# Performance work log

Hardware: AMD Instinct MI355X
Metric: run time of the kernel (lower is better)

Reference implementation:

```python
import jax, jax.numpy as jnp
import numpy as np

# ---- static config (matches init_kwargs / langevin args) ----
B, N, D = 2, 16384, 3
F_DIM = 128      # feature_net.out_channels
H_DIM = 128      # score_net hidden
N_BLOCKS = 2
K = 4            # denoise_knn
NUM_STEPS = 4
STEP_SIZE = 0.2
STEP_DECAY = 0.95

# static sliding-window neighbor indices, computed once (numpy -> constant)
_offsets = np.arange(-(K - 1) // 2, (K - 1) // 2 + 1)
NBR_IDX = np.clip(np.arange(N)[:, None] + _offsets, 0, N - 1)   # (N, K)
NBR_FLAT = NBR_IDX.reshape(-1)                                  # (N*K,)


def setup_inputs() -> dict:
    key = jax.random.key(0)
    ks = jax.random.split(key, 8)
    s = 0.05
    return {
        "pcl_noisy": jax.random.normal(ks[0], (B, N, D), jnp.float32),
        "Wf1": jax.random.normal(ks[1], (D, F_DIM), jnp.float32) * s,
        "bf1": jnp.zeros((F_DIM,), jnp.float32),
        "Wf2": jax.random.normal(ks[2], (F_DIM, F_DIM), jnp.float32) * s,
        "bf2": jnp.zeros((F_DIM,), jnp.float32),
        "W0": jax.random.normal(ks[3], (D + F_DIM, H_DIM), jnp.float32) * s,
        "b0": jnp.zeros((H_DIM,), jnp.float32),
        "Wb": jax.random.normal(ks[4], (N_BLOCKS, H_DIM, H_DIM), jnp.float32) * s,
        "bb": jnp.zeros((N_BLOCKS, H_DIM), jnp.float32),
        "Wo": jax.random.normal(ks[5], (H_DIM, D), jnp.float32) * s,
        "bo": jnp.zeros((D,), jnp.float32),
    }


def _feature_net(pcl, Wf1, bf1, Wf2, bf2):
    # pointwise MLP: (B,N,3) -> (B,N,F)
    h = jax.nn.relu(pcl @ Wf1 + bf1)
    return h @ Wf2 + bf2


def _score_net(x_cent, feat, W0, b0, Wb, bb, Wo, bo):
    # x_cent: (B,N,K,3) centered frames, feat: (B,N,F) per-seed context
    c = jnp.broadcast_to(feat[:, :, None, :], x_cent.shape[:3] + (feat.shape[-1],))
    h = jax.nn.relu(jnp.concatenate([x_cent, c], axis=-1) @ W0 + b0)  # (B,N,K,H)
    for i in range(N_BLOCKS):  # small fixed residual stack
        h = h + jax.nn.relu(h @ Wb[i] + bb[i])
    return h @ Wo + bo  # (B,N,K,3)


def reference(pcl_noisy, Wf1, bf1, Wf2, bf2, W0, b0, Wb, bb, Wo, bo):
    feat = _feature_net(pcl_noisy, Wf1, bf1, Wf2, bf2)  # (B,N,F), computed once

    def step(pcl_next, step_i):
        frames = pcl_next[:, NBR_IDX, :]                      # gather (B,N,K,3)
        centered = frames - pcl_noisy[:, :, None, :]          # center on original cloud
        grad_pred = _score_net(centered, feat, W0, b0, Wb, bb, Wo, bo)  # (B,N,K,3)
        acc = jnp.zeros_like(pcl_noisy).at[:, NBR_FLAT, :].add(
            grad_pred.reshape(pcl_noisy.shape[0], -1, D))     # scatter_add (B,N,3)
        s = STEP_SIZE * (STEP_DECAY ** step_i.astype(jnp.float32))
        return pcl_next + s * acc, None

    pcl_next, _ = jax.lax.scan(step, pcl_noisy, jnp.arange(NUM_STEPS))
    return pcl_next
```

## Files before the change

kernel.cpp:

```cpp
#include <hip/hip_runtime.h>
#include <hip/hip_bf16.h>

#define NPT    16384
#define TOTP   32768
#define FD     128
#define CHK    32
#define CPB    (NPT/CHK)
#define GRID   (2*CPB)
#define EXT    (CHK+24)
#define FQM    (CHK+21)

#define OFF_WFA 0
#define OFF_WFB 16384
#define OFF_WB  32768
#define OFF_WO  98304
#define PREP_TOT 100352

typedef unsigned short u16;
typedef __attribute__((ext_vector_type(8))) short bf16x8;
typedef __attribute__((ext_vector_type(4))) float f32x4;

__device__ __forceinline__ float bf2f(u16 u) {
    union { unsigned int i; float f; } v; v.i = ((unsigned int)u) << 16; return v.f;
}
__device__ __forceinline__ u16 f2bf(float f) {
    union { float f; unsigned int i; } v; v.f = f;
    unsigned int u = v.i;
    u = u + 0x7FFFu + ((u >> 16) & 1u);
    return (u16)(u >> 16);
}
__device__ __forceinline__ u16 f2bf_hw(float f) {
    __hip_bfloat16 h = __float2bfloat16(f);
    return *(u16*)&h;
}
__device__ __forceinline__ int swz(int row, int colbyte) {
    return row*256 + (colbyte ^ ((row & 7) << 4));
}
__device__ __forceinline__ int fswz(int row, int col) {
    return row*256 + ((col*2) ^ ((row & 7) << 4));
}

__global__ __launch_bounds__(256) void prep_weights(
    const float* __restrict__ Wf2, const float* __restrict__ W0,
    const float* __restrict__ Wb,  const float* __restrict__ Wo,
    u16* __restrict__ W)
{
    int t = blockIdx.x*256 + threadIdx.x;
    if (t >= PREP_TOT) return;
    float val;
    if (t < OFF_WB) {
        int u = t & 16383;
        int e = u & 7, l = (u >> 3) & 63, kk = (u >> 9) & 3;
        int ntg = (u >> 11) & 1, wid = (u >> 12) & 3;
        int col = wid*32 + ntg*16 + (l & 15);
        int k   = kk*32 + (l >> 4)*8 + e;
        val = (t < OFF_WFB) ? Wf2[k*FD + col] : W0[(3+k)*FD + col];
    } else if (t < OFF_WO) {
        int u = t - OFF_WB;
        int e = u & 7, l = (u >> 3) & 63, kk = (u >> 9) & 3;
        int ntg = (u >> 11) & 1, layer = (u >> 12) & 1, wid = (u >> 13) & 3;
        int col = wid*32 + ntg*16 + (l & 15);
        int k   = kk*32 + (l >> 4)*8 + e;
        val = Wb[layer*FD*FD + k*FD + col];
    } else {
        int u = t - OFF_WO;
        int e = u & 7, l = (u >> 3) & 63, kk = (u >> 9) & 3;
        int l15 = l & 15;
        int k   = kk*32 + (l >> 4)*8 + e;
        val = (l15 < 3) ? Wo[k*3 + l15] : 0.f;
    }
    W[t] = f2bf(val);
}

__global__ __launch_bounds__(256, 2) void fused_all(
    const float* __restrict__ pcl, const float* __restrict__ Wf1,
    const float* __restrict__ bf1, const float* __restrict__ bf2,
    const float* __restrict__ W0,  const float* __restrict__ b0,
    const float* __restrict__ bb,  const float* __restrict__ bo,
    const u16* __restrict__ Wprep, float* __restrict__ out)
{
    __shared__ __align__(16) u16   fpl[FQM*128];
    __shared__ __align__(16) float X0l[EXT*3];
    __shared__ __align__(16) float Xal[EXT*3];
    __shared__ __align__(16) float Xbl[EXT*3];
    __shared__ __align__(16) char  hA[8192];
    __shared__ __align__(16) char  hB[8192];
    __shared__ __align__(16) char  hC[8192];

    const int tid = threadIdx.x, wid = tid >> 6, l = tid & 63;
    const int l15 = l & 15, l4 = l >> 4;
    const int colb = wid * 32;

    const int blk = blockIdx.x;
    const int b = blk >> 9, cidx = blk & (CPB - 1);
    const int A = cidx * CHK;
    const int Bp = A + CHK - 1;
    const int elo  = (A - 12 < 0) ? 0 : A - 12;
    const int ehi  = (Bp + 12 > NPT-1) ? NPT-1 : Bp + 12;
    const int esz3 = (ehi - elo + 1) * 3;
    const int fqlo = (A - 10 < 0) ? 0 : A - 10;
    const int fqhi = (Bp + 11 > NPT-1) ? NPT-1 : Bp + 11;
    const int fqc  = fqhi - fqlo + 1;
    const size_t gb = (size_t)b * NPT;

    for (int i = tid; i < esz3; i += 256) X0l[i] = pcl[(gb + elo)*3 + i];
    __syncthreads();

    {
        bf16x8 wfA[2][4], wfB[2][4];
        {
            const bf16x8* fa = (const bf16x8*)(Wprep + OFF_WFA);
            const bf16x8* fb = (const bf16x8*)(Wprep + OFF_WFB);
            #pragma unroll
            for (int ntg = 0; ntg < 2; ++ntg)
                #pragma unroll
                for (int kk = 0; kk < 4; ++kk) {
                    int fi = ((wid*2 + ntg)*4 + kk)*64 + l;
                    wfA[ntg][kk] = fa[fi];
                    wfB[ntg][kk] = fb[fi];
                }
        }
        float wf1c[3][2], bf1v[2], bf2v[2], b0v[2];
        #pragma unroll
        for (int ntg = 0; ntg < 2; ++ntg) {
            int col = colb + ntg*16 + l15;
            wf1c[0][ntg] = Wf1[0*FD+col];
            wf1c[1][ntg] = Wf1[1*FD+col];
            wf1c[2][ntg] = Wf1[2*FD+col];
            bf1v[ntg] = bf1[col]; bf2v[ntg] = bf2[col]; b0v[ntg] = b0[col];
        }
        const int nft = (fqc + 31) >> 5;
        for (int ft = 0; ft < nft; ++ft) {
            const int r0 = ft*32;
            #pragma unroll
            for (int rt = 0; rt < 2; ++rt)
                #pragma unroll
                for (int reg = 0; reg < 4; ++reg) {
                    int row = rt*16 + l4*4 + reg;
                    int q = fqlo + r0 + row; if (q > fqhi) q = fqhi;
                    int qe = (q - elo)*3;
                    float px = X0l[qe], py = X0l[qe+1], pz = X0l[qe+2];
                    #pragma unroll
                    for (int ntg = 0; ntg < 2; ++ntg) {
                        float tv = bf1v[ntg] + px*wf1c[0][ntg] + py*wf1c[1][ntg] + pz*wf1c[2][ntg];
                        tv = fmaxf(tv, 0.f);
                        int col = colb + ntg*16 + l15;
                        *(u16*)(hA + swz(row, col*2)) = f2bf_hw(tv);
                    }
                }
            __syncthreads();
            {
                bf16x8 a[2][4];
                #pragma unroll
                for (int rt = 0; rt < 2; ++rt)
                    #pragma unroll
                    for (int kk = 0; kk < 4; ++kk)
                        a[rt][kk] = *(const bf16x8*)(hA + swz(rt*16 + l15, kk*64 + l4*16));
                #pragma unroll
                for (int ntg = 0; ntg < 2; ++ntg) {
                    f32x4 acc0 = {bf2v[ntg],bf2v[ntg],bf2v[ntg],bf2v[ntg]};
                    f32x4 acc1 = acc0;
                    #pragma unroll
                    for (int kk = 0; kk < 4; ++kk) {
                        acc0 = __builtin_amdgcn_mfma_f32_16x16x32_bf16(a[0][kk], wfA[ntg][kk], acc0, 0,0,0);
                        acc1 = __builtin_amdgcn_mfma_f32_16x16x32_bf16(a[1][kk], wfA[ntg][kk], acc1, 0,0,0);
                    }
                    int col = colb + ntg*16 + l15;
                    #pragma unroll
                    for (int reg = 0; reg < 4; ++reg) {
                        *(u16*)(hB + swz(l4*4+reg,    col*2)) = f2bf_hw(acc0[reg]);
                        *(u16*)(hB + swz(16+l4*4+reg, col*2)) = f2bf_hw(acc1[reg]);
                    }
                }
            }
            __syncthreads();
            {
                bf16x8 a[2][4];
                #pragma unroll
                for (int rt = 0; rt < 2; ++rt)
                    #pragma unroll
                    for (int kk = 0; kk < 4; ++kk)
                        a[rt][kk] = *(const bf16x8*)(hB + swz(rt*16 + l15, kk*64 + l4*16));
                #pragma unroll
                for (int ntg = 0; ntg < 2; ++ntg) {
                    f32x4 acc0 = {b0v[ntg],b0v[ntg],b0v[ntg],b0v[ntg]};
                    f32x4 acc1 = acc0;
                    #pragma unroll
                    for (int kk = 0; kk < 4; ++kk) {
                        acc0 = __builtin_amdgcn_mfma_f32_16x16x32_bf16(a[0][kk], wfB[ntg][kk], acc0, 0,0,0);
                        acc1 = __builtin_amdgcn_mfma_f32_16x16x32_bf16(a[1][kk], wfB[ntg][kk], acc1, 0,0,0);
                    }
                    int col = colb + ntg*16 + l15;
                    #pragma unroll
                    for (int reg = 0; reg < 4; ++reg) {
                        int ra = r0 + l4*4 + reg, rb = r0 + 16 + l4*4 + reg;
                        if (ra < fqc) *(u16*)((char*)fpl + fswz(ra, col)) = f2bf_hw(acc0[reg]);
                        if (rb < fqc) *(u16*)((char*)fpl + fswz(rb, col)) = f2bf_hw(acc1[reg]);
                    }
                }
            }
            __syncthreads();
        }
    }
    __builtin_amdgcn_sched_barrier(0);

    bf16x8 wfrag[2][2][4], wofrag[4];
    {
        const bf16x8* wb = (const bf16x8*)(Wprep + OFF_WB);
        #pragma unroll
        for (int layer = 0; layer < 2; ++layer)
            #pragma unroll
            for (int ntg = 0; ntg < 2; ++ntg)
                #pragma unroll
                for (int kk = 0; kk < 4; ++kk)
                    wfrag[layer][ntg][kk] = wb[(((wid*2+layer)*2+ntg)*4+kk)*64 + l];
        const bf16x8* wo = (const bf16x8*)(Wprep + OFF_WO);
        #pragma unroll
        for (int kk = 0; kk < 4; ++kk) wofrag[kk] = wo[kk*64 + l];
    }
    float w0c[3][2], bbv[2][2];
    #pragma unroll
    for (int ntg = 0; ntg < 2; ++ntg) {
        int col = colb + ntg*16 + l15;
        w0c[0][ntg] = W0[0*FD+col];
        w0c[1][ntg] = W0[1*FD+col];
        w0c[2][ntg] = W0[2*FD+col];
        bbv[0][ntg] = bb[col]; bbv[1][ntg] = bb[FD+col];
    }
    const float bol = (l15 < 3) ? bo[l15] : 0.f;

    auto do_step = [&](const float* curl, float* nxtl, float sval, int qlo, int qhi) {
        for (int i = tid; i < esz3; i += 256) nxtl[i] = curl[i];
        __syncthreads();
        const int nt_ = (qhi - qlo + 8) >> 3;
        for (int t = 0; t < nt_; ++t) {
            const int qbase = qlo + t*8;
            float hc[2][2][4];
            #pragma unroll
            for (int rt = 0; rt < 2; ++rt) {
                int q = qbase + rt*4 + l4; if (q > qhi) q = qhi;
                int qe = (q - elo)*3;
                float nx = X0l[qe], ny = X0l[qe+1], nz = X0l[qe+2];
                float cx[4], cy[4], cz[4];
                #pragma unroll
                for (int k = 0; k < 4; ++k) {
                    int nb = q + k - 2;
                    nb = nb < 0 ? 0 : (nb > NPT-1 ? NPT-1 : nb);
                    int te = (nb - elo)*3;
                    cx[k] = curl[te]   - nx;
                    cy[k] = curl[te+1] - ny;
                    cz[k] = curl[te+2] - nz;
                }
                #pragma unroll
                for (int ntg = 0; ntg < 2; ++ntg) {
                    int col = colb + ntg*16 + l15;
                    float fp = bf2f(*(const u16*)((const char*)fpl + fswz(q - fqlo, col)));
                    #pragma unroll
                    for (int reg = 0; reg < 4; ++reg) {
                        float u = fp + cx[reg]*w0c[0][ntg] + cy[reg]*w0c[1][ntg] + cz[reg]*w0c[2][ntg];
                        u = fmaxf(u, 0.f);
                        hc[rt][ntg][reg] = u;
                        *(u16*)(hA + swz(rt*16 + l4*4 + reg, col*2)) = f2bf_hw(u);
                    }
                }
            }
            __syncthreads();
            {
                bf16x8 a[2][4];
                #pragma unroll
                for (int rt = 0; rt < 2; ++rt)
                    #pragma unroll
                    for (int kk = 0; kk < 4; ++kk)
                        a[rt][kk] = *(const bf16x8*)(hA + swz(rt*16 + l15, kk*64 + l4*16));
                #pragma unroll
                for (int ntg = 0; ntg < 2; ++ntg) {
                    f32x4 acc0 = {bbv[0][ntg],bbv[0][ntg],bbv[0][ntg],bbv[0][ntg]};
                    f32x4 acc1 = acc0;
                    #pragma unroll
                    for (int kk = 0; kk < 4; ++kk) {
                        acc0 = __builtin_amdgcn_mfma_f32_16x16x32_bf16(a[0][kk], wfrag[0][ntg][kk], acc0, 0,0,0);
                        acc1 = __builtin_amdgcn_mfma_f32_16x16x32_bf16(a[1][kk], wfrag[0][ntg][kk], acc1, 0,0,0);
                    }
                    int col = colb + ntg*16 + l15;
                    #pragma unroll
                    for (int reg = 0; reg < 4; ++reg) {
                        hc[0][ntg][reg] += fmaxf(acc0[reg], 0.f);
                        hc[1][ntg][reg] += fmaxf(acc1[reg], 0.f);
                        *(u16*)(hB + swz(l4*4+reg,    col*2)) = f2bf_hw(hc[0][ntg][reg]);
                        *(u16*)(hB + swz(16+l4*4+reg, col*2)) = f2bf_hw(hc[1][ntg][reg]);
                    }
                }
            }
            __syncthreads();
            {
                bf16x8 a[2][4];
                #pragma unroll
                for (int rt = 0; rt < 2; ++rt)
                    #pragma unroll
                    for (int kk = 0; kk < 4; ++kk)
                        a[rt][kk] = *(const bf16x8*)(hB + swz(rt*16 + l15, kk*64 + l4*16));
                #pragma unroll
                for (int ntg = 0; ntg < 2; ++ntg) {
                    f32x4 acc0 = {bbv[1][ntg],bbv[1][ntg],bbv[1][ntg],bbv[1][ntg]};
                    f32x4 acc1 = acc0;
                    #pragma unroll
                    for (int kk = 0; kk < 4; ++kk) {
                        acc0 = __builtin_amdgcn_mfma_f32_16x16x32_bf16(a[0][kk], wfrag[1][ntg][kk], acc0, 0,0,0);
                        acc1 = __builtin_amdgcn_mfma_f32_16x16x32_bf16(a[1][kk], wfrag[1][ntg][kk], acc1, 0,0,0);
                    }
                    int col = colb + ntg*16 + l15;
                    #pragma unroll
                    for (int reg = 0; reg < 4; ++reg) {
                        float h0 = hc[0][ntg][reg] + fmaxf(acc0[reg], 0.f);
                        float h1 = hc[1][ntg][reg] + fmaxf(acc1[reg], 0.f);
                        *(u16*)(hC + swz(l4*4+reg,    col*2)) = f2bf_hw(h0);
                        *(u16*)(hC + swz(16+l4*4+reg, col*2)) = f2bf_hw(h1);
                    }
                }
            }
            __syncthreads();
            if (wid < 2) {
                const int sub = wid;
                bf16x8 a[4];
                #pragma unroll
                for (int kk = 0; kk < 4; ++kk)
                    a[kk] = *(const bf16x8*)(hC + swz(sub*16 + l15, kk*64 + l4*16));
                f32x4 acc = {0.f,0.f,0.f,0.f};
                #pragma unroll
                for (int kk = 0; kk < 4; ++kk)
                    acc = __builtin_amdgcn_mfma_f32_16x16x32_bf16(a[kk], wofrag[kk], acc, 0,0,0);
                int q = qbase + sub*4 + l4;
                if (l15 < 3 && q <= qhi) {
                    #pragma unroll
                    for (int reg = 0; reg < 4; ++reg) {
                        int nb = q + reg - 2;
                        nb = nb < 0 ? 0 : (nb > NPT-1 ? NPT-1 : nb);
                        atomicAdd(&nxtl[(nb - elo)*3 + l15], sval*(acc[reg] + bol));
                    }
                }
            }
        }
        __syncthreads();
    };

    const int q1lo = fqlo,                 q1hi = fqhi;
    const int q2lo = (A-7 < 0) ? 0 : A-7,  q2hi = (Bp+8 > NPT-1) ? NPT-1 : Bp+8;
    const int q3lo = (A-4 < 0) ? 0 : A-4,  q3hi = (Bp+5 > NPT-1) ? NPT-1 : Bp+5;
    const int q4lo = (A-1 < 0) ? 0 : A-1,  q4hi = (Bp+2 > NPT-1) ? NPT-1 : Bp+2;

    do_step(X0l, Xal, 0.2f,      q1lo, q1hi);
    do_step(Xal, Xbl, 0.19f,     q2lo, q2hi);
    do_step(Xbl, Xal, 0.1805f,   q3lo, q3hi);
    do_step(Xal, Xbl, 0.171475f, q4lo, q4hi);

    for (int i = tid; i < CHK*3; i += 256)
        out[(gb + A)*3 + i] = Xbl[(A - elo)*3 + i];
}

extern "C" void kernel_launch(void* const* d_in, const int* in_sizes, int n_in,
                              void* d_out, int out_size, void* d_ws, size_t ws_size,
                              hipStream_t stream) {
    const float* pcl = (const float*)d_in[0];
    const float* Wf1 = (const float*)d_in[1];
    const float* bf1 = (const float*)d_in[2];
    const float* Wf2 = (const float*)d_in[3];
    const float* bf2 = (const float*)d_in[4];
    const float* W0  = (const float*)d_in[5];
    const float* b0  = (const float*)d_in[6];
    const float* Wb  = (const float*)d_in[7];
    const float* bb  = (const float*)d_in[8];
    const float* Wo  = (const float*)d_in[9];
    const float* bo  = (const float*)d_in[10];
    float* out = (float*)d_out;

    u16* Wprep = (u16*)d_ws;

    prep_weights<<<(PREP_TOT+255)/256, 256, 0, stream>>>(Wf2, W0, Wb, Wo, Wprep);
    fused_all<<<GRID, 256, 0, stream>>>(pcl, Wf1, bf1, bf2, W0, b0, bb, bo, Wprep, out);
}
```

Before: 198.2 us.

## Double chunk size and process two score-net tiles per barrier

Doubles the per-block chunk of points, reducing the redundant halo recomputation of features and earlier Langevin steps. Inside each step, two 8-point tiles are processed between each pair of barriers using duplicated LDS buffers, halving synchronizations and letting all four waves do the output projection. The cost is more LDS per block and fewer blocks in the grid, which may reduce occupancy and load balance.

```diff
diff --git a/kernel.cpp b/kernel.cpp
--- a/kernel.cpp
+++ b/kernel.cpp
@@ -4,7 +4,7 @@
 #define NPT    16384
 #define TOTP   32768
 #define FD     128
-#define CHK    32
+#define CHK    64
 #define CPB    (NPT/CHK)
 #define GRID   (2*CPB)
 #define EXT    (CHK+24)
@@ -83,16 +83,19 @@
     __shared__ __align__(16) float X0l[EXT*3];
     __shared__ __align__(16) float Xal[EXT*3];
     __shared__ __align__(16) float Xbl[EXT*3];
-    __shared__ __align__(16) char  hA[8192];
-    __shared__ __align__(16) char  hB[8192];
-    __shared__ __align__(16) char  hC[8192];
+    __shared__ __align__(16) char  hA0[8192];
+    __shared__ __align__(16) char  hA1[8192];
+    __shared__ __align__(16) char  hB0[8192];
+    __shared__ __align__(16) char  hB1[8192];
+    __shared__ __align__(16) char  hC0[8192];
+    __shared__ __align__(16) char  hC1[8192];
 
     const int tid = threadIdx.x, wid = tid >> 6, l = tid & 63;
     const int l15 = l & 15, l4 = l >> 4;
     const int colb = wid * 32;
 
     const int blk = blockIdx.x;
-    const int b = blk >> 9, cidx = blk & (CPB - 1);
+    const int b = blk >> 8, cidx = blk & (CPB - 1);
     const int A = cidx * CHK;
     const int Bp = A + CHK - 1;
     const int elo  = (A - 12 < 0) ? 0 : A - 12;
@@ -145,7 +148,7 @@
                         float tv = bf1v[ntg] + px*wf1c[0][ntg] + py*wf1c[1][ntg] + pz*wf1c[2][ntg];
                         tv = fmaxf(tv, 0.f);
                         int col = colb + ntg*16 + l15;
-                        *(u16*)(hA + swz(row, col*2)) = f2bf_hw(tv);
+                        *(u16*)(hA0 + swz(row, col*2)) = f2bf_hw(tv);
                     }
                 }
             __syncthreads();
@@ -155,7 +158,7 @@
                 for (int rt = 0; rt < 2; ++rt)
                     #pragma unroll
                     for (int kk = 0; kk < 4; ++kk)
-                        a[rt][kk] = *(const bf16x8*)(hA + swz(rt*16 + l15, kk*64 + l4*16));
+                        a[rt][kk] = *(const bf16x8*)(hA0 + swz(rt*16 + l15, kk*64 + l4*16));
                 #pragma unroll
                 for (int ntg = 0; ntg < 2; ++ntg) {
                     f32x4 acc0 = {bf2v[ntg],bf2v[ntg],bf2v[ntg],bf2v[ntg]};
@@ -168,8 +171,8 @@
                     int col = colb + ntg*16 + l15;
                     #pragma unroll
                     for (int reg = 0; reg < 4; ++reg) {
-                        *(u16*)(hB + swz(l4*4+reg,    col*2)) = f2bf_hw(acc0[reg]);
-                        *(u16*)(hB + swz(16+l4*4+reg, col*2)) = f2bf_hw(acc1[reg]);
+                        *(u16*)(hB0 + swz(l4*4+reg,    col*2)) = f2bf_hw(acc0[reg]);
+                        *(u16*)(hB0 + swz(16+l4*4+reg, col*2)) = f2bf_hw(acc1[reg]);
                     }
                 }
             }
@@ -180,7 +183,7 @@
                 for (int rt = 0; rt < 2; ++rt)
                     #pragma unroll
                     for (int kk = 0; kk < 4; ++kk)
-                        a[rt][kk] = *(const bf16x8*)(hB + swz(rt*16 + l15, kk*64 + l4*16));
+                        a[rt][kk] = *(const bf16x8*)(hB0 + swz(rt*16 + l15, kk*64 + l4*16));
                 #pragma unroll
                 for (int ntg = 0; ntg < 2; ++ntg) {
                     f32x4 acc0 = {b0v[ntg],b0v[ntg],b0v[ntg],b0v[ntg]};
@@ -232,10 +235,8 @@
     auto do_step = [&](const float* curl, float* nxtl, float sval, int qlo, int qhi) {
         for (int i = tid; i < esz3; i += 256) nxtl[i] = curl[i];
         __syncthreads();
-        const int nt_ = (qhi - qlo + 8) >> 3;
-        for (int t = 0; t < nt_; ++t) {
-            const int qbase = qlo + t*8;
-            float hc[2][2][4];
+
+        auto layer0 = [&](char* hAt, int qbase, float (&hc)[2][2][4]) {
             #pragma unroll
             for (int rt = 0; rt < 2; ++rt) {
                 int q = qbase + rt*4 + l4; if (q > qhi) q = qhi;
@@ -260,76 +261,93 @@
                         float u = fp + cx[reg]*w0c[0][ntg] + cy[reg]*w0c[1][ntg] + cz[reg]*w0c[2][ntg];
                         u = fmaxf(u, 0.f);
                         hc[rt][ntg][reg] = u;
-                        *(u16*)(hA + swz(rt*16 + l4*4 + reg, col*2)) = f2bf_hw(u);
-                    }
-                }
-            }
+                        *(u16*)(hAt + swz(rt*16 + l4*4 + reg, col*2)) = f2bf_hw(u);
+                    }
+                }
+            }
+        };
+        auto layer1 = [&](const char* hAt, char* hBt, float (&hc)[2][2][4]) {
+            bf16x8 a[2][4];
+            #pragma unroll
+            for (int rt = 0; rt < 2; ++rt)
+                #pragma unroll
+                for (int kk = 0; kk < 4; ++kk)
+                    a[rt][kk] = *(const bf16x8*)(hAt + swz(rt*16 + l15, kk*64 + l4*16));
+            #pragma unroll
+            for (int ntg = 0; ntg < 2; ++ntg) {
+                f32x4 acc0 = {bbv[0][ntg],bbv[0][ntg],bbv[0][ntg],bbv[0][ntg]};
+                f32x4 acc1 = acc0;
+                #pragma unroll
+                for (int kk = 0; kk < 4; ++kk) {
+                    acc0 = __builtin_amdgcn_mfma_f32_16x16x32_bf16(a[0][kk], wfrag[0][ntg][kk], acc0, 0,0,0);
+                    acc1 = __builtin_amdgcn_mfma_f32_16x16x32_bf16(a[1][kk], wfrag[0][ntg][kk], acc1, 0,0,0);
+                }
+                int col = colb + ntg*16 + l15;
+                #pragma unroll
+                for (int reg = 0; reg < 4; ++reg) {
+                    hc[0][ntg][reg] += fmaxf(acc0[reg], 0.f);
+                    hc[1][ntg][reg] += fmaxf(acc1[reg], 0.f);
+                    *(u16*)(hBt + swz(l4*4+reg,    col*2)) = f2bf_hw(hc[0][ntg][reg]);
+                    *(u16*)(hBt + swz(16+l4*4+reg, col*2)) = f2bf_hw(hc[1][ntg][reg]);
+                }
+            }
+        };
+        auto layer2 = [&](const char* hBt, char* hCt, float (&hc)[2][2][4]) {
+            bf16x8 a[2][4];
+            #pragma unroll
+            for (int rt = 0; rt < 2; ++rt)
+                #pragma unroll
+                for (int kk = 0; kk < 4; ++kk)
+                    a[rt][kk] = *(const bf16x8*)(hBt + swz(rt*16 + l15, kk*64 + l4*16));
+            #pragma unroll
+            for (int ntg = 0; ntg < 2; ++ntg) {
+                f32x4 acc0 = {bbv[1][ntg],bbv[1][ntg],bbv[1][ntg],bbv[1][ntg]};
+                f32x4 acc1 = acc0;
+                #pragma unroll
+                for (int kk = 0; kk < 4; ++kk) {
+                    acc0 = __builtin_amdgcn_mfma_f32_16x16x32_bf16(a[0][kk], wfrag[1][ntg][kk], acc0, 0,0,0);
+                    acc1 = __builtin_amdgcn_mfma_f32_16x16x32_bf16(a[1][kk], wfrag[1][ntg][kk], acc1, 0,0,0);
+                }
+                int col = colb + ntg*16 + l15;
+                #pragma unroll
+                for (int reg = 0; reg < 4; ++reg) {
+                    float h0 = hc[0][ntg][reg] + fmaxf(acc0[reg], 0.f);
+                    float h1 = hc[1][ntg][reg] + fmaxf(acc1[reg], 0.f);
+                    *(u16*)(hCt + swz(l4*4+reg,    col*2)) = f2bf_hw(h0);
+                    *(u16*)(hCt + swz(16+l4*4+reg, col*2)) = f2bf_hw(h1);
+                }
+            }
+        };
+
+        const int nt_ = (qhi - qlo + 8) >> 3;
+        const int ng_ = (nt_ + 1) >> 1;
+        for (int g = 0; g < ng_; ++g) {
+            const int qb0 = qlo + (g*2)*8;
+            const int qb1 = qlo + (g*2+1)*8;
+            const bool has1 = (g*2+1) < nt_;
+            float hc0[2][2][4], hc1[2][2][4];
+            layer0(hA0, qb0, hc0);
+            if (has1) layer0(hA1, qb1, hc1);
+            __syncthreads();
+            layer1(hA0, hB0, hc0);
+            if (has1) layer1(hA1, hB1, hc1);
+            __syncthreads();
+            layer2(hB0, hC0, hc0);
+            if (has1) layer2(hB1, hC1, hc1);
             __syncthreads();
             {
-                bf16x8 a[2][4];
-                #pragma unroll
-                for (int rt = 0; rt < 2; ++rt)
-                    #pragma unroll
-                    for (int kk = 0; kk < 4; ++kk)
-                        a[rt][kk] = *(const bf16x8*)(hA + swz(rt*16 + l15, kk*64 + l4*16));
-                #pragma unroll
-                for (int ntg = 0; ntg < 2; ++ntg) {
-                    f32x4 acc0 = {bbv[0][ntg],bbv[0][ntg],bbv[0][ntg],bbv[0][ntg]};
-                    f32x4 acc1 = acc0;
-                    #pragma unroll
-                    for (int kk = 0; kk < 4; ++kk) {
-                        acc0 = __builtin_amdgcn_mfma_f32_16x16x32_bf16(a[0][kk], wfrag[0][ntg][kk], acc0, 0,0,0);
-                        acc1 = __builtin_amdgcn_mfma_f32_16x16x32_bf16(a[1][kk], wfrag[0][ntg][kk], acc1, 0,0,0);
-                    }
-                    int col = colb + ntg*16 + l15;
-                    #pragma unroll
-                    for (int reg = 0; reg < 4; ++reg) {
-                        hc[0][ntg][reg] += fmaxf(acc0[reg], 0.f);
-                        hc[1][ntg][reg] += fmaxf(acc1[reg], 0.f);
-                        *(u16*)(hB + swz(l4*4+reg,    col*2)) = f2bf_hw(hc[0][ntg][reg]);
-                        *(u16*)(hB + swz(16+l4*4+reg, col*2)) = f2bf_hw(hc[1][ntg][reg]);
-                    }
-                }
-            }
-            __syncthreads();
-            {
-                bf16x8 a[2][4];
-                #pragma unroll
-                for (int rt = 0; rt < 2; ++rt)
-                    #pragma unroll
-                    for (int kk = 0; kk < 4; ++kk)
-                        a[rt][kk] = *(const bf16x8*)(hB + swz(rt*16 + l15, kk*64 + l4*16));
-                #pragma unroll
-                for (int ntg = 0; ntg < 2; ++ntg) {
-                    f32x4 acc0 = {bbv[1][ntg],bbv[1][ntg],bbv[1][ntg],bbv[1][ntg]};
-                    f32x4 acc1 = acc0;
-                    #pragma unroll
-                    for (int kk = 0; kk < 4; ++kk) {
-                        acc0 = __builtin_amdgcn_mfma_f32_16x16x32_bf16(a[0][kk], wfrag[1][ntg][kk], acc0, 0,0,0);
-                        acc1 = __builtin_amdgcn_mfma_f32_16x16x32_bf16(a[1][kk], wfrag[1][ntg][kk], acc1, 0,0,0);
-                    }
-                    int col = colb + ntg*16 + l15;
-                    #pragma unroll
-                    for (int reg = 0; reg < 4; ++reg) {
-                        float h0 = hc[0][ntg][reg] + fmaxf(acc0[reg], 0.f);
-                        float h1 = hc[1][ntg][reg] + fmaxf(acc1[reg], 0.f);
-                        *(u16*)(hC + swz(l4*4+reg,    col*2)) = f2bf_hw(h0);
-                        *(u16*)(hC + swz(16+l4*4+reg, col*2)) = f2bf_hw(h1);
-                    }
-                }
-            }
-            __syncthreads();
-            if (wid < 2) {
-                const int sub = wid;
+                const int t = wid >> 1, sub = wid & 1;
+                const char* hCt = t ? hC1 : hC0;
+                const int qb = t ? qb1 : qb0;
                 bf16x8 a[4];
                 #pragma unroll
                 for (int kk = 0; kk < 4; ++kk)
-                    a[kk] = *(const bf16x8*)(hC + swz(sub*16 + l15, kk*64 + l4*16));
+                    a[kk] = *(const bf16x8*)(hCt + swz(sub*16 + l15, kk*64 + l4*16));
                 f32x4 acc = {0.f,0.f,0.f,0.f};
                 #pragma unroll
                 for (int kk = 0; kk < 4; ++kk)
                     acc = __builtin_amdgcn_mfma_f32_16x16x32_bf16(a[kk], wofrag[kk], acc, 0,0,0);
-                int q = qbase + sub*4 + l4;
+                int q = qb + sub*4 + l4;
                 if (l15 < 3 && q <= qhi) {
                     #pragma unroll
                     for (int reg = 0; reg < 4; ++reg) {
```

Result: faster. 174.5 us (-12.0%).
